# Optimization experiments

Hardware: AMD Instinct MI355X
Metric: run time of the kernel (lower is better)

The kernel has to match this reference:

```python
import jax, jax.numpy as jnp
import numpy as np

D_NODE, D_EDGE, D_HEAD = 256, 128, 32
LN_EPS = 1e-5


def setup_inputs() -> dict:
    key = jax.random.key(0)
    ks = jax.random.split(key, 10)
    B, N = 1, 512
    s_node = 1.0 / np.sqrt(D_NODE)
    s_hh = 1.0 / np.sqrt(D_HEAD * D_HEAD)
    return {
        "node": jax.random.normal(ks[0], (B, N, D_NODE), dtype=jnp.float32),
        "edge": jax.random.normal(ks[1], (B, N, N, D_EDGE), dtype=jnp.float32),
        "ln_w": jnp.ones((D_NODE,), dtype=jnp.float32),
        "ln_b": jnp.zeros((D_NODE,), dtype=jnp.float32),
        "w_left": jax.random.normal(ks[2], (D_NODE, D_HEAD), dtype=jnp.float32) * s_node,
        "b_left": jax.random.normal(ks[3], (D_HEAD,), dtype=jnp.float32) * 0.02,
        "w_right": jax.random.normal(ks[4], (D_NODE, D_HEAD), dtype=jnp.float32) * s_node,
        "b_right": jax.random.normal(ks[5], (D_HEAD,), dtype=jnp.float32) * 0.02,
        "w_out": jax.random.normal(ks[6], (D_HEAD * D_HEAD, D_EDGE), dtype=jnp.float32) * s_hh,
        "b_out": jax.random.normal(ks[7], (D_EDGE,), dtype=jnp.float32) * 0.02,
    }


def reference(node, edge, ln_w, ln_b, w_left, b_left, w_right, b_right, w_out, b_out):
    # LayerNorm over d_node
    mu = jnp.mean(node, axis=-1, keepdims=True)
    var = jnp.mean(jnp.square(node - mu), axis=-1, keepdims=True)
    x = (node - mu) * jax.lax.rsqrt(var + LN_EPS) * ln_w + ln_b

    left = x @ w_left + b_left    # [B, N, d_head]
    right = x @ w_right + b_right  # [B, N, d_head]

    # Outer product flattened over (i,j) then projected to d_edge.
    # Fused: reshape w_out to [i, j, e] and contract directly, avoiding the
    # explicit [B, N, N, d_head*d_head] intermediate (same math as
    # einsum('bni,bmj->bnmij').flatten(-2) @ w_out).
    w3 = w_out.reshape(D_HEAD, D_HEAD, D_EDGE)
    out = jnp.einsum("bni,bmj,ije->bnme", left, right, w3) + b_out
    return out + edge
```

## Files before the change

### kernel.cpp

```cpp
#include <hip/hip_runtime.h>

#define D_NODE 256
#define D_EDGE 128
#define D_HEAD 32
#define NN 512

__global__ __launch_bounds__(256) void ln_proj_kernel(
    const float* __restrict__ node, const float* __restrict__ ln_w,
    const float* __restrict__ ln_b, const float* __restrict__ w_left,
    const float* __restrict__ b_left, const float* __restrict__ w_right,
    const float* __restrict__ b_right, float* __restrict__ leftT,
    float* __restrict__ right) {
  __shared__ float xs[D_NODE];
  __shared__ float red[10];
  __shared__ float part[4][64];
  const int n = blockIdx.x;
  const int t = threadIdx.x;
  float v = node[n * D_NODE + t];
  float s = v, ss = v * v;
#pragma unroll
  for (int o = 32; o > 0; o >>= 1) {
    s += __shfl_down(s, o);
    ss += __shfl_down(ss, o);
  }
  if ((t & 63) == 0) {
    red[t >> 6] = s;
    red[4 + (t >> 6)] = ss;
  }
  __syncthreads();
  if (t == 0) {
    float S = red[0] + red[1] + red[2] + red[3];
    float SS = red[4] + red[5] + red[6] + red[7];
    float mu = S * (1.0f / D_NODE);
    float var = SS * (1.0f / D_NODE) - mu * mu;
    red[8] = mu;
    red[9] = rsqrtf(var + 1e-5f);
  }
  __syncthreads();
  const float mu = red[8], rs = red[9];
  xs[t] = (v - mu) * rs * ln_w[t] + ln_b[t];
  __syncthreads();
  {
    const int col = t & 63;
    const int q = t >> 6;
    const int c = col & 31;
    const float* w = (col < 32) ? w_left : w_right;
    float acc = 0.f;
    const int d0 = q * 64;
#pragma unroll 8
    for (int d = d0; d < d0 + 64; ++d) acc = fmaf(xs[d], w[d * D_HEAD + c], acc);
    part[q][col] = acc;
  }
  __syncthreads();
  if (t < 64) {
    const int c = t & 31;
    const bool isL = (t < 32);
    float acc = part[0][t] + part[1][t] + part[2][t] + part[3][t] +
                (isL ? b_left[c] : b_right[c]);
    if (isL)
      leftT[c * NN + n] = acc;
    else
      right[n * D_HEAD + c] = acc;
  }
}

__global__ __launch_bounds__(256) void rw_kernel(
    const float* __restrict__ right, const float* __restrict__ w_out,
    float* __restrict__ tmp) {
  const int m = blockIdx.x;
  const int t = threadIdx.x;
  const int e4 = t & 31;
  const int i8 = t >> 5;
  const float* r = right + m * D_HEAD;
#pragma unroll
  for (int k = 0; k < 4; ++k) {
    const int i = i8 * 4 + k;
    const float4* wp = (const float4*)(w_out + i * D_HEAD * D_EDGE) + e4;
    float4 a = {0.f, 0.f, 0.f, 0.f};
#pragma unroll
    for (int j = 0; j < D_HEAD; ++j) {
      const float4 w4 = wp[j * (D_EDGE / 4)];
      const float rj = r[j];
      a.x = fmaf(rj, w4.x, a.x);
      a.y = fmaf(rj, w4.y, a.y);
      a.z = fmaf(rj, w4.z, a.z);
      a.w = fmaf(rj, w4.w, a.w);
    }
    ((float4*)(tmp + (m * D_HEAD + i) * D_EDGE))[e4] = a;
  }
}

__global__ __launch_bounds__(256) void fuse_kernel(
    const float* __restrict__ leftT, const float* __restrict__ tmp,
    const float* __restrict__ b_out, const float* __restrict__ edge,
    float* __restrict__ out) {
  const int m = blockIdx.x;
  const int wave = __builtin_amdgcn_readfirstlane(threadIdx.x >> 6);
  const int lane = threadIdx.x & 63;
  const int nbase = blockIdx.y * 32 + wave * 8;

  const float2* tp = (const float2*)(tmp + m * D_HEAD * D_EDGE) + lane;
  const float2 be = ((const float2*)b_out)[lane];
  const float2* edge2 = (const float2*)edge;
  float2* out2 = (float2*)out;
  const long rowstride = (long)NN * (D_EDGE / 2);
  const long base = ((long)nbase * NN + m) * (D_EDGE / 2) + lane;

  float2 ed[8];
#pragma unroll
  for (int r = 0; r < 8; ++r) ed[r] = edge2[base + r * rowstride];

  float2 acc[8];
#pragma unroll
  for (int r = 0; r < 8; ++r) acc[r] = be;

  const float* lB = leftT + nbase;
#pragma unroll
  for (int i = 0; i < D_HEAD; ++i) {
    const float2 rt = tp[i * (D_EDGE / 2)];
#pragma unroll
    for (int r = 0; r < 8; ++r) {
      const float l = lB[i * NN + r];
      acc[r].x = fmaf(l, rt.x, acc[r].x);
      acc[r].y = fmaf(l, rt.y, acc[r].y);
    }
  }
#pragma unroll
  for (int r = 0; r < 8; ++r) {
    acc[r].x += ed[r].x;
    acc[r].y += ed[r].y;
    out2[base + r * rowstride] = acc[r];
  }
}

extern "C" void kernel_launch(void* const* d_in, const int* in_sizes, int n_in,
                              void* d_out, int out_size, void* d_ws, size_t ws_size,
                              hipStream_t stream) {
  const float* node    = (const float*)d_in[0];
  const float* edge    = (const float*)d_in[1];
  const float* ln_w    = (const float*)d_in[2];
  const float* ln_b    = (const float*)d_in[3];
  const float* w_left  = (const float*)d_in[4];
  const float* b_left  = (const float*)d_in[5];
  const float* w_right = (const float*)d_in[6];
  const float* b_right = (const float*)d_in[7];
  const float* w_out   = (const float*)d_in[8];
  const float* b_out   = (const float*)d_in[9];
  float* out = (float*)d_out;

  float* leftT = (float*)d_ws;
  float* right = leftT + D_HEAD * NN;
  float* tmp   = right + NN * D_HEAD;

  ln_proj_kernel<<<NN, 256, 0, stream>>>(node, ln_w, ln_b, w_left, b_left,
                                         w_right, b_right, leftT, right);
  rw_kernel<<<NN, 256, 0, stream>>>(right, w_out, tmp);
  fuse_kernel<<<dim3(NN, 16), 256, 0, stream>>>(leftT, tmp, b_out, edge, out);
}
```

Measured before the change: 280.8 us.

## Restructure fuse kernel with LDS-staged tmp, float4 tiles and edge prefetch

The fuse kernel now stages the tmp slices for two m columns in shared memory. Each wave loops over four groups of 8 rows with float4 accumulators, double-buffers the edge loads for the next group in registers, and writes output with nontemporal stores. The left projection is stored row-major so each row's coefficients sit together. rw_kernel is retiled so each thread reuses one w_out load across 4 m values. These changes target the memory-bound 128MB edge read and output write, at the cost of higher register pressure and 32KB of LDS per block.

```diff
diff --git a/kernel.cpp b/kernel.cpp
--- a/kernel.cpp
+++ b/kernel.cpp
@@ -5,11 +5,13 @@
 #define D_HEAD 32
 #define NN 512
 
+typedef float f4v __attribute__((ext_vector_type(4)));
+
 __global__ __launch_bounds__(256) void ln_proj_kernel(
     const float* __restrict__ node, const float* __restrict__ ln_w,
     const float* __restrict__ ln_b, const float* __restrict__ w_left,
     const float* __restrict__ b_left, const float* __restrict__ w_right,
-    const float* __restrict__ b_right, float* __restrict__ leftT,
+    const float* __restrict__ b_right, float* __restrict__ left,
     float* __restrict__ right) {
   __shared__ float xs[D_NODE];
   __shared__ float red[10];
@@ -57,79 +59,103 @@
     const bool isL = (t < 32);
     float acc = part[0][t] + part[1][t] + part[2][t] + part[3][t] +
                 (isL ? b_left[c] : b_right[c]);
-    if (isL)
-      leftT[c * NN + n] = acc;
-    else
-      right[n * D_HEAD + c] = acc;
+    (isL ? left : right)[n * D_HEAD + c] = acc;
   }
 }
 
 __global__ __launch_bounds__(256) void rw_kernel(
     const float* __restrict__ right, const float* __restrict__ w_out,
     float* __restrict__ tmp) {
-  const int m = blockIdx.x;
-  const int t = threadIdx.x;
-  const int e4 = t & 31;
-  const int i8 = t >> 5;
-  const float* r = right + m * D_HEAD;
+  const int m0 = blockIdx.x * 4;
+  const int i = blockIdx.y * 8 + (threadIdx.x >> 5);
+  const int e4 = threadIdx.x & 31;
+  const float4* wp = (const float4*)(w_out + i * D_HEAD * D_EDGE) + e4;
+  const float* r = right + m0 * D_HEAD;
+  float4 a0 = {0, 0, 0, 0}, a1 = {0, 0, 0, 0}, a2 = {0, 0, 0, 0},
+         a3 = {0, 0, 0, 0};
 #pragma unroll
-  for (int k = 0; k < 4; ++k) {
-    const int i = i8 * 4 + k;
-    const float4* wp = (const float4*)(w_out + i * D_HEAD * D_EDGE) + e4;
-    float4 a = {0.f, 0.f, 0.f, 0.f};
-#pragma unroll
-    for (int j = 0; j < D_HEAD; ++j) {
-      const float4 w4 = wp[j * (D_EDGE / 4)];
-      const float rj = r[j];
-      a.x = fmaf(rj, w4.x, a.x);
-      a.y = fmaf(rj, w4.y, a.y);
-      a.z = fmaf(rj, w4.z, a.z);
-      a.w = fmaf(rj, w4.w, a.w);
-    }
-    ((float4*)(tmp + (m * D_HEAD + i) * D_EDGE))[e4] = a;
+  for (int j = 0; j < D_HEAD; ++j) {
+    const float4 w4 = wp[j * (D_EDGE / 4)];
+    const float r0 = r[j], r1 = r[32 + j], r2 = r[64 + j], r3 = r[96 + j];
+    a0.x = fmaf(r0, w4.x, a0.x); a0.y = fmaf(r0, w4.y, a0.y);
+    a0.z = fmaf(r0, w4.z, a0.z); a0.w = fmaf(r0, w4.w, a0.w);
+    a1.x = fmaf(r1, w4.x, a1.x); a1.y = fmaf(r1, w4.y, a1.y);
+    a1.z = fmaf(r1, w4.z, a1.z); a1.w = fmaf(r1, w4.w, a1.w);
+    a2.x = fmaf(r2, w4.x, a2.x); a2.y = fmaf(r2, w4.y, a2.y);
+    a2.z = fmaf(r2, w4.z, a2.z); a2.w = fmaf(r2, w4.w, a2.w);
+    a3.x = fmaf(r3, w4.x, a3.x); a3.y = fmaf(r3, w4.y, a3.y);
+    a3.z = fmaf(r3, w4.z, a3.z); a3.w = fmaf(r3, w4.w, a3.w);
   }
+  ((float4*)(tmp + ((m0 + 0) * D_HEAD + i) * D_EDGE))[e4] = a0;
+  ((float4*)(tmp + ((m0 + 1) * D_HEAD + i) * D_EDGE))[e4] = a1;
+  ((float4*)(tmp + ((m0 + 2) * D_HEAD + i) * D_EDGE))[e4] = a2;
+  ((float4*)(tmp + ((m0 + 3) * D_HEAD + i) * D_EDGE))[e4] = a3;
 }
 
 __global__ __launch_bounds__(256) void fuse_kernel(
-    const float* __restrict__ leftT, const float* __restrict__ tmp,
+    const float* __restrict__ left, const float* __restrict__ tmp,
     const float* __restrict__ b_out, const float* __restrict__ edge,
     float* __restrict__ out) {
-  const int m = blockIdx.x;
-  const int wave = __builtin_amdgcn_readfirstlane(threadIdx.x >> 6);
-  const int lane = threadIdx.x & 63;
-  const int nbase = blockIdx.y * 32 + wave * 8;
+  __shared__ float tl[2 * D_HEAD * D_EDGE];
+  const int m0 = blockIdx.x * 2;
+  const int t = threadIdx.x;
+  {
+    const float4* ts = (const float4*)(tmp + m0 * D_HEAD * D_EDGE);
+    float4* td = (float4*)tl;
+#pragma unroll
+    for (int k = 0; k < 8; ++k) td[t + 256 * k] = ts[t + 256 * k];
+  }
+  const int lane = t & 63;
+  const int wv = __builtin_amdgcn_readfirstlane(t >> 6);
+  const int e4 = lane & 31;
+  const int mh = lane >> 5;
+  const int n0 = blockIdx.y * 128 + wv * 32;
+  const float4 be = ((const float4*)b_out)[e4];
+  const float* tb = tl + mh * (D_HEAD * D_EDGE) + e4 * 4;
+  const float4* edge4 = (const float4*)edge;
+  float4* out4 = (float4*)out;
+  const int rowstr = NN * (D_EDGE / 4);
+  const int base = (n0 * NN + m0) * (D_EDGE / 4) + lane;
 
-  const float2* tp = (const float2*)(tmp + m * D_HEAD * D_EDGE) + lane;
-  const float2 be = ((const float2*)b_out)[lane];
-  const float2* edge2 = (const float2*)edge;
-  float2* out2 = (float2*)out;
-  const long rowstride = (long)NN * (D_EDGE / 2);
-  const long base = ((long)nbase * NN + m) * (D_EDGE / 2) + lane;
+  float4 eb[2][8];
+#pragma unroll
+  for (int r = 0; r < 8; ++r) eb[0][r] = edge4[base + r * rowstr];
+  __syncthreads();
 
-  float2 ed[8];
 #pragma unroll
-  for (int r = 0; r < 8; ++r) ed[r] = edge2[base + r * rowstride];
-
-  float2 acc[8];
+  for (int g = 0; g < 4; ++g) {
+    const int cur = g & 1;
+    const int gb = base + g * 8 * rowstr;
+    if (g < 3) {
 #pragma unroll
-  for (int r = 0; r < 8; ++r) acc[r] = be;
-
-  const float* lB = leftT + nbase;
+      for (int r = 0; r < 8; ++r)
+        eb[cur ^ 1][r] = edge4[gb + (8 + r) * rowstr];
+    }
+    float4 acc[8];
 #pragma unroll
-  for (int i = 0; i < D_HEAD; ++i) {
-    const float2 rt = tp[i * (D_EDGE / 2)];
+    for (int r = 0; r < 8; ++r) acc[r] = be;
+    const float* lp = left + (n0 + g * 8) * D_HEAD;
+#pragma unroll 4
+    for (int i = 0; i < D_HEAD; ++i) {
+      const float4 tv = *(const float4*)(tb + i * D_EDGE);
+#pragma unroll
+      for (int r = 0; r < 8; ++r) {
+        const float l = lp[r * D_HEAD + i];
+        acc[r].x = fmaf(l, tv.x, acc[r].x);
+        acc[r].y = fmaf(l, tv.y, acc[r].y);
+        acc[r].z = fmaf(l, tv.z, acc[r].z);
+        acc[r].w = fmaf(l, tv.w, acc[r].w);
+      }
+    }
 #pragma unroll
     for (int r = 0; r < 8; ++r) {
-      const float l = lB[i * NN + r];
-      acc[r].x = fmaf(l, rt.x, acc[r].x);
-      acc[r].y = fmaf(l, rt.y, acc[r].y);
+      acc[r].x += eb[cur][r].x;
+      acc[r].y += eb[cur][r].y;
+      acc[r].z += eb[cur][r].z;
+      acc[r].w += eb[cur][r].w;
+      __builtin_nontemporal_store(*(const f4v*)&acc[r],
+                                  (f4v*)(out4 + gb + r * rowstr));
     }
-  }
-#pragma unroll
-  for (int r = 0; r < 8; ++r) {
-    acc[r].x += ed[r].x;
-    acc[r].y += ed[r].y;
-    out2[base + r * rowstride] = acc[r];
   }
 }
 
@@ -148,12 +174,12 @@
   const float* b_out   = (const float*)d_in[9];
   float* out = (float*)d_out;
 
-  float* leftT = (float*)d_ws;
-  float* right = leftT + D_HEAD * NN;
+  float* left  = (float*)d_ws;
+  float* right = left + NN * D_HEAD;
   float* tmp   = right + NN * D_HEAD;
 
   ln_proj_kernel<<<NN, 256, 0, stream>>>(node, ln_w, ln_b, w_left, b_left,
-                                         w_right, b_right, leftT, right);
-  rw_kernel<<<NN, 256, 0, stream>>>(right, w_out, tmp);
-  fuse_kernel<<<dim3(NN, 16), 256, 0, stream>>>(leftT, tmp, b_out, edge, out);
+                                         w_right, b_right, left, right);
+  rw_kernel<<<dim3(NN / 4, 4), 256, 0, stream>>>(right, w_out, tmp);
+  fuse_kernel<<<dim3(NN / 2, 4), 256, 0, stream>>>(left, tmp, b_out, edge, out);
 }
```

New measurement: 271.9 us. 3.2% less time.
